# Kernel tuning notes

Hardware: AMD Instinct MI355X
Metric: run time of the kernel (lower is better)

## Reference

```python
import jax, jax.numpy as jnp
import numpy as np

N_NODES = 100000
N_EDGES = 1600000
NFEAT, NHID, NCLASS = 256, 256, 64
NLAYERS = 4


def _gcn_norm(edge_index, n_nodes):
    # PyG GCNConv default: add self-loops, symmetric normalization
    src, dst = edge_index[0], edge_index[1]
    loop = jnp.arange(n_nodes, dtype=edge_index.dtype)
    src = jnp.concatenate([src, loop])
    dst = jnp.concatenate([dst, loop])
    deg = jax.ops.segment_sum(jnp.ones_like(dst, dtype=jnp.float32), dst,
                              num_segments=n_nodes)
    dinv = jnp.where(deg > 0, jax.lax.rsqrt(deg), 0.0)
    norm = dinv[src] * dinv[dst]  # [E+N]
    return src, dst, norm


def _gcn_layer(X, W, b, src, dst, norm, n_nodes):
    H = X @ W                      # [N, out]
    msg = H[src] * norm[:, None]   # [E+N, out] gather + scale
    out = jax.ops.segment_sum(msg, dst, num_segments=n_nodes)
    return out + b


def setup_inputs() -> dict:
    key = jax.random.key(0)
    ks = jax.random.split(key, 8)
    x = jax.random.normal(ks[0], (N_NODES, NFEAT), dtype=jnp.float32)
    edge_index = jax.random.randint(ks[1], (2, N_EDGES), 0, N_NODES, dtype=jnp.int32)
    def glorot(k, fan_in, fan_out):
        s = jnp.sqrt(6.0 / (fan_in + fan_out))
        return jax.random.uniform(k, (fan_in, fan_out), jnp.float32, -s, s)
    return {
        "x": x,
        "W_enc": glorot(ks[2], NFEAT, NHID),
        "b_enc": jnp.zeros((NHID,), jnp.float32),
        "W_conv": glorot(ks[3], NHID, NHID),
        "b_conv": jnp.zeros((NHID,), jnp.float32),
        "W_dec": glorot(ks[4], NHID, NCLASS),
        "b_dec": jnp.zeros((NCLASS,), jnp.float32),
        "edge_index": edge_index,
    }


def reference(x, W_enc, b_enc, W_conv, b_conv, W_dec, b_dec, edge_index):
    n_nodes = x.shape[0]
    src, dst, norm = _gcn_norm(edge_index, n_nodes)
    # dropout probs are 0 (drop_in=drop=0) -> identity
    X = jax.nn.relu(_gcn_layer(x, W_enc, b_enc, src, dst, norm, n_nodes))
    for _ in range(NLAYERS):
        X = jax.nn.relu(_gcn_layer(X, W_conv, b_conv, src, dst, norm, n_nodes))
    X = jax.nn.relu(_gcn_layer(X, W_dec, b_dec, src, dst, norm, n_nodes))
    return X
```

## Files before the change

### kernel.cpp

```cpp
#include <hip/hip_runtime.h>

#define N_NODES 100000
#define N_EDGES 1600000
#define MPAD    100096
#define NB_SCAN ((N_NODES + 255) / 256)

using short8  = __attribute__((ext_vector_type(8))) short;
using ushort8 = __attribute__((ext_vector_type(8))) unsigned short;
using f32x4   = __attribute__((ext_vector_type(4))) float;

__device__ inline unsigned short f2bf(float f) {
    unsigned u = __float_as_uint(f);
    unsigned r = (u + 0x7fffu + ((u >> 16) & 1u)) >> 16;
    return (unsigned short)r;
}
__device__ inline float bf2f(unsigned short h) {
    return __uint_as_float(((unsigned)h) << 16);
}


__global__ __launch_bounds__(256) void k_init(int* __restrict__ indeg,
                                              int* __restrict__ cursor, int n) {
    int i = blockIdx.x * blockDim.x + threadIdx.x;
    if (i < n) { indeg[i] = 0; cursor[i] = 0; }
}

__global__ __launch_bounds__(256) void k_indeg(const int* __restrict__ dst,
                                               int* __restrict__ indeg, int e) {
    int i = blockIdx.x * blockDim.x + threadIdx.x;
    if (i < e) atomicAdd(&indeg[dst[i]], 1);
}

__global__ __launch_bounds__(256) void k_scan_blocks(const int* __restrict__ indeg,
                                                     int* __restrict__ blksum, int n) {
    int i = blockIdx.x * 256 + threadIdx.x;
    int v = (i < n) ? indeg[i] : 0;
#pragma unroll
    for (int o = 32; o > 0; o >>= 1) v += __shfl_down(v, o, 64);
    __shared__ int ws[4];
    if ((threadIdx.x & 63) == 0) ws[threadIdx.x >> 6] = v;
    __syncthreads();
    if (threadIdx.x == 0) blksum[blockIdx.x] = ws[0] + ws[1] + ws[2] + ws[3];
}

__global__ __launch_bounds__(512) void k_scan_top(const int* __restrict__ blksum,
                                                  int* __restrict__ blkpref,
                                                  int* __restrict__ offsets, int nb, int n) {
    __shared__ int s[512];
    int t = threadIdx.x;
    int v = (t < nb) ? blksum[t] : 0;
    s[t] = v;
    __syncthreads();
    for (int o = 1; o < 512; o <<= 1) {
        int u = (t >= o) ? s[t - o] : 0;
        __syncthreads();
        s[t] += u;
        __syncthreads();
    }
    if (t < nb) blkpref[t] = (t == 0) ? 0 : s[t - 1];
    if (t == nb - 1) offsets[n] = s[t];
}

__global__ __launch_bounds__(256) void k_scan_final(const int* __restrict__ indeg,
                                                    const int* __restrict__ blkpref,
                                                    int* __restrict__ offsets,
                                                    float* __restrict__ dinv, int n) {
    __shared__ int s[256];
    int t = threadIdx.x;
    int i = blockIdx.x * 256 + t;
    int v = (i < n) ? indeg[i] : 0;
    s[t] = v;
    __syncthreads();
    for (int o = 1; o < 256; o <<= 1) {
        int u = (t >= o) ? s[t - o] : 0;
        __syncthreads();
        s[t] += u;
        __syncthreads();
    }
    if (i < n) {
        offsets[i] = blkpref[blockIdx.x] + s[t] - v;
        dinv[i] = rsqrtf((float)(v + 1));
    }
}

__global__ __launch_bounds__(256) void k_scatter(const int* __restrict__ src,
                                                 const int* __restrict__ dst,
                                                 const float* __restrict__ dinv,
                                                 const int* __restrict__ offsets,
                                                 int* __restrict__ cursor,
                                                 int* __restrict__ csr_src,
                                                 float* __restrict__ csr_norm, int e) {
    int i = blockIdx.x * blockDim.x + threadIdx.x;
    if (i < e) {
        int d = dst[i], s = src[i];
        int pos = offsets[d] + atomicAdd(&cursor[d], 1);
        csr_src[pos] = s;
        csr_norm[pos] = dinv[s] * dinv[d];
    }
}


__global__ __launch_bounds__(256) void k_cvt_x(const float* __restrict__ x,
                                               unsigned short* __restrict__ xb) {
    int i = blockIdx.x * blockDim.x + threadIdx.x;
    int row = i >> 6;
    ushort4 o;
    if (row < N_NODES) {
        float4 v = *(const float4*)(x + (size_t)i * 4);
        o.x = f2bf(v.x); o.y = f2bf(v.y); o.z = f2bf(v.z); o.w = f2bf(v.w);
    } else {
        o.x = o.y = o.z = o.w = 0;
    }
    *(ushort4*)(xb + (size_t)i * 4) = o;
}

__global__ __launch_bounds__(256) void k_prep_w(const float* __restrict__ W,
                                                unsigned short* __restrict__ Wt, int N) {
    int i = blockIdx.x * blockDim.x + threadIdx.x;
    if (i < 256 * N) {
        int r = i / N, c = i - r * N;
        Wt[(size_t)c * 256 + r] = f2bf(W[i]);
    }
}


template <int BN>
__global__ __launch_bounds__(256) void k_mfma_gemm(const unsigned short* __restrict__ A,
                                                   const unsigned short* __restrict__ Bt,
                                                   unsigned short* __restrict__ C,
                                                   int Ntot) {
    constexpr int K = 256, BK = 64;
    constexpr int NFR = BN / 32;
    __shared__ char ldsA[128 * 128];
    __shared__ char ldsB[BN * 128];
    const int tid  = threadIdx.x;
    const int lane = tid & 63;
    const int wid  = tid >> 6;
    const int wr   = wid >> 1, wc = wid & 1;
    const int row0 = blockIdx.x * 128;
    const int col0 = blockIdx.y * BN;
    const int l15  = lane & 15, lhi = lane >> 4;

    f32x4 acc[4][NFR];
#pragma unroll
    for (int m = 0; m < 4; ++m)
#pragma unroll
        for (int n = 0; n < NFR; ++n) acc[m][n] = {0.f, 0.f, 0.f, 0.f};

    for (int k0 = 0; k0 < K; k0 += BK) {
#pragma unroll
        for (int j = 0; j < 4; ++j) {
            int ci = j * 256 + tid;
            int r = ci >> 3;
            int cb = (ci & 7) ^ (r & 7);
            const char* src = (const char*)(A + (size_t)(row0 + r) * K + k0) + cb * 16;
            __builtin_amdgcn_global_load_lds((const __attribute__((address_space(1))) void*)src,
                                             (__attribute__((address_space(3))) void*)(ldsA + ci * 16),
                                             16, 0, 0);
        }
#pragma unroll
        for (int j = 0; j < BN / 32; ++j) {
            int ci = j * 256 + tid;
            int r = ci >> 3;
            int cb = (ci & 7) ^ (r & 7);
            const char* src = (const char*)(Bt + (size_t)(col0 + r) * K + k0) + cb * 16;
            __builtin_amdgcn_global_load_lds((const __attribute__((address_space(1))) void*)src,
                                             (__attribute__((address_space(3))) void*)(ldsB + ci * 16),
                                             16, 0, 0);
        }
        __syncthreads();
#pragma unroll
        for (int kk = 0; kk < 2; ++kk) {
            short8 af[4], bfr[NFR];
            int cb = kk * 4 + lhi;
#pragma unroll
            for (int m = 0; m < 4; ++m) {
                int r = wr * 64 + m * 16 + l15;
                af[m] = *(const short8*)(ldsA + r * 128 + ((cb ^ (r & 7)) << 4));
            }
#pragma unroll
            for (int n = 0; n < NFR; ++n) {
                int r = wc * (NFR * 16) + n * 16 + l15;
                bfr[n] = *(const short8*)(ldsB + r * 128 + ((cb ^ (r & 7)) << 4));
            }
#pragma unroll
            for (int m = 0; m < 4; ++m)
#pragma unroll
                for (int n = 0; n < NFR; ++n)
                    acc[m][n] = __builtin_amdgcn_mfma_f32_16x16x32_bf16(af[m], bfr[n],
                                                                        acc[m][n], 0, 0, 0);
        }
        __syncthreads();
    }
#pragma unroll
    for (int m = 0; m < 4; ++m)
#pragma unroll
        for (int n = 0; n < NFR; ++n) {
            int col = col0 + wc * (NFR * 16) + n * 16 + l15;
            int rbase = row0 + wr * 64 + m * 16 + lhi * 4;
#pragma unroll
            for (int q = 0; q < 4; ++q)
                C[(size_t)(rbase + q) * Ntot + col] = f2bf(acc[m][n][q]);
        }
}


__global__ __launch_bounds__(256) void k_agg256(const unsigned short* __restrict__ H,
                                                const int* __restrict__ offsets,
                                                const int* __restrict__ csr_src,
                                                const float* __restrict__ csr_norm,
                                                const float* __restrict__ dinv,
                                                const float* __restrict__ bias,
                                                unsigned short* __restrict__ out, int n) {
    const int wid = __builtin_amdgcn_readfirstlane((blockIdx.x * blockDim.x + threadIdx.x) >> 6);
    if (wid >= n) return;
    const int lane = threadIdx.x & 63;
    const int half = lane >> 5;
    const unsigned coff = (unsigned)(lane & 31) * 16u;

    float acc[8] = {};
    const int beg = offsets[wid], end = offsets[wid + 1];
    int e = beg;

    auto do_pair = [&](int ea) {
        int s0 = csr_src[ea], s1 = csr_src[ea + 1];
        float n0 = csr_norm[ea], n1 = csr_norm[ea + 1];
        unsigned off = (unsigned)(half ? s1 : s0) * 512u + coff;
        float nrm = half ? n1 : n0;
        ushort8 v = *(const ushort8*)((const char*)H + off);
#pragma unroll
        for (int j = 0; j < 8; ++j) acc[j] = fmaf(bf2f(v[j]), nrm, acc[j]);
    };

    for (; e + 3 < end; e += 4) { do_pair(e); do_pair(e + 2); }
    for (; e + 1 < end; e += 2) { do_pair(e); }

    {
        float dv = dinv[wid];
        float sw = dv * dv;
        int  has_tail = (e < end);
        int   sA = has_tail ? csr_src[e]  : wid;
        float nA = has_tail ? csr_norm[e] : sw;
        float nB = has_tail ? sw : 0.f;
        unsigned off = (unsigned)(half ? wid : sA) * 512u + coff;
        float nrm = half ? nB : nA;
        ushort8 v = *(const ushort8*)((const char*)H + off);
#pragma unroll
        for (int j = 0; j < 8; ++j) acc[j] = fmaf(bf2f(v[j]), nrm, acc[j]);
    }

#pragma unroll
    for (int j = 0; j < 8; ++j) acc[j] += __shfl_xor(acc[j], 32);

    if (half == 0) {
        const float* bp = bias + (lane & 31) * 8;
        float4 b0 = *(const float4*)bp;
        float4 b1 = *(const float4*)(bp + 4);
        ushort8 o;
        o[0] = f2bf(fmaxf(acc[0] + b0.x, 0.f));
        o[1] = f2bf(fmaxf(acc[1] + b0.y, 0.f));
        o[2] = f2bf(fmaxf(acc[2] + b0.z, 0.f));
        o[3] = f2bf(fmaxf(acc[3] + b0.w, 0.f));
        o[4] = f2bf(fmaxf(acc[4] + b1.x, 0.f));
        o[5] = f2bf(fmaxf(acc[5] + b1.y, 0.f));
        o[6] = f2bf(fmaxf(acc[6] + b1.z, 0.f));
        o[7] = f2bf(fmaxf(acc[7] + b1.w, 0.f));
        *(ushort8*)((char*)out + (unsigned)wid * 512u + coff) = o;
    }
}


__global__ __launch_bounds__(256) void k_agg64(const unsigned short* __restrict__ H,
                                               const int* __restrict__ offsets,
                                               const int* __restrict__ csr_src,
                                               const float* __restrict__ csr_norm,
                                               const float* __restrict__ dinv,
                                               const float* __restrict__ bias,
                                               float* __restrict__ out, int n) {
    const int wid = __builtin_amdgcn_readfirstlane((blockIdx.x * blockDim.x + threadIdx.x) >> 6);
    if (wid >= n) return;
    const int lane = threadIdx.x & 63;
    const int q = lane >> 4;
    const unsigned coff = (unsigned)(lane & 15) * 8u;

    float acc[4] = {};
    const int beg = offsets[wid], end = offsets[wid + 1];
    int e = beg;

    for (; e + 3 < end; e += 4) {
        int s0 = csr_src[e], s1 = csr_src[e + 1], s2 = csr_src[e + 2], s3 = csr_src[e + 3];
        float n0 = csr_norm[e], n1 = csr_norm[e + 1], n2 = csr_norm[e + 2], n3 = csr_norm[e + 3];
        int srow = s0; float nrm = n0;
        if (q == 1) { srow = s1; nrm = n1; }
        else if (q == 2) { srow = s2; nrm = n2; }
        else if (q == 3) { srow = s3; nrm = n3; }
        ushort4 v = *(const ushort4*)((const char*)H + (unsigned)srow * 128u + coff);
        acc[0] = fmaf(bf2f(v.x), nrm, acc[0]);
        acc[1] = fmaf(bf2f(v.y), nrm, acc[1]);
        acc[2] = fmaf(bf2f(v.z), nrm, acc[2]);
        acc[3] = fmaf(bf2f(v.w), nrm, acc[3]);
    }
    {
        float dv = dinv[wid];
        float sw = dv * dv;
        int r = end - e;
        int srow = wid; float nrm = 0.f;
        if (q < r) { srow = csr_src[e + q]; nrm = csr_norm[e + q]; }
        else if (q == r) { srow = wid; nrm = sw; }
        ushort4 v = *(const ushort4*)((const char*)H + (unsigned)srow * 128u + coff);
        acc[0] = fmaf(bf2f(v.x), nrm, acc[0]);
        acc[1] = fmaf(bf2f(v.y), nrm, acc[1]);
        acc[2] = fmaf(bf2f(v.z), nrm, acc[2]);
        acc[3] = fmaf(bf2f(v.w), nrm, acc[3]);
    }
#pragma unroll
    for (int j = 0; j < 4; ++j) {
        acc[j] += __shfl_xor(acc[j], 16);
        acc[j] += __shfl_xor(acc[j], 32);
    }
    if (q == 0) {
        float4 b = *(const float4*)(bias + (lane & 15) * 4);
        float4 o = make_float4(fmaxf(acc[0] + b.x, 0.f), fmaxf(acc[1] + b.y, 0.f),
                               fmaxf(acc[2] + b.z, 0.f), fmaxf(acc[3] + b.w, 0.f));
        *(float4*)((char*)out + (size_t)wid * 256u + coff * 2u) = o;
    }
}


extern "C" void kernel_launch(void* const* d_in, const int* in_sizes, int n_in,
                              void* d_out, int out_size, void* d_ws, size_t ws_size,
                              hipStream_t stream) {
    const float* x      = (const float*)d_in[0];
    const float* W_enc  = (const float*)d_in[1];
    const float* b_enc  = (const float*)d_in[2];
    const float* W_conv = (const float*)d_in[3];
    const float* b_conv = (const float*)d_in[4];
    const float* W_dec  = (const float*)d_in[5];
    const float* b_dec  = (const float*)d_in[6];
    const int*   ei     = (const int*)d_in[7];

    const int N = N_NODES;
    const int E = N_EDGES;
    const int* src = ei;
    const int* dst = ei + E;

    size_t off = 0;
    auto carve = [&](size_t bytes) -> void* {
        void* p = (char*)d_ws + off;
        off = (off + bytes + 255) & ~(size_t)255;
        return p;
    };
    unsigned short* Xb      = (unsigned short*)carve((size_t)MPAD * 256 * 2);
    unsigned short* Hb      = (unsigned short*)carve((size_t)MPAD * 256 * 2);
    unsigned short* Wt_enc  = (unsigned short*)carve((size_t)256 * 256 * 2);
    unsigned short* Wt_conv = (unsigned short*)carve((size_t)256 * 256 * 2);
    unsigned short* Wt_dec  = (unsigned short*)carve((size_t)64 * 256 * 2);
    int*            indeg   = (int*)carve((size_t)N * sizeof(int));
    int*            cursor  = (int*)carve((size_t)N * sizeof(int));
    float*          dinv    = (float*)carve((size_t)N * sizeof(float));
    int*            offsets = (int*)carve((size_t)(N + 1) * sizeof(int));
    int*            csr_src = (int*)carve((size_t)E * sizeof(int));
    float*          csr_nrm = (float*)carve((size_t)E * sizeof(float));
    int*            blksum  = (int*)carve((size_t)NB_SCAN * sizeof(int));
    int*            blkpref = (int*)carve((size_t)NB_SCAN * sizeof(int));
    (void)ws_size;

    k_cvt_x<<<MPAD / 4, 256, 0, stream>>>(x, Xb);
    k_prep_w<<<(256 * 256 + 255) / 256, 256, 0, stream>>>(W_enc, Wt_enc, 256);
    k_prep_w<<<(256 * 256 + 255) / 256, 256, 0, stream>>>(W_conv, Wt_conv, 256);
    k_prep_w<<<(256 * 64 + 255) / 256, 256, 0, stream>>>(W_dec, Wt_dec, 64);
    k_init<<<(N + 255) / 256, 256, 0, stream>>>(indeg, cursor, N);
    k_indeg<<<(E + 255) / 256, 256, 0, stream>>>(dst, indeg, E);
    k_scan_blocks<<<NB_SCAN, 256, 0, stream>>>(indeg, blksum, N);
    k_scan_top<<<1, 512, 0, stream>>>(blksum, blkpref, offsets, NB_SCAN, N);
    k_scan_final<<<NB_SCAN, 256, 0, stream>>>(indeg, blkpref, offsets, dinv, N);
    k_scatter<<<(E + 255) / 256, 256, 0, stream>>>(src, dst, dinv, offsets, cursor,
                                                   csr_src, csr_nrm, E);

    dim3 gconv(MPAD / 128, 2);
    dim3 gdec(MPAD / 128, 1);
    const int agg_blocks = (N + 3) / 4;

    k_mfma_gemm<128><<<gconv, 256, 0, stream>>>(Xb, Wt_enc, Hb, 256);
    k_agg256<<<agg_blocks, 256, 0, stream>>>(Hb, offsets, csr_src, csr_nrm, dinv, b_enc, Xb, N);
    for (int l = 0; l < 4; ++l) {
        k_mfma_gemm<128><<<gconv, 256, 0, stream>>>(Xb, Wt_conv, Hb, 256);
        k_agg256<<<agg_blocks, 256, 0, stream>>>(Hb, offsets, csr_src, csr_nrm, dinv, b_conv, Xb, N);
    }
    k_mfma_gemm<64><<<gdec, 256, 0, stream>>>(Xb, Wt_dec, Hb, 64);
    k_agg64<<<agg_blocks, 256, 0, stream>>>(Hb, offsets, csr_src, csr_nrm, dinv, b_dec,
                                            (float*)d_out, N);
}
```

Measured before the change: 1.033 ms.

## Factor symmetric GCN norm into GEMM epilogue and aggregation, drop per-edge norm array

Splits the per-edge weight dinv[s]*dinv[d] into a row scale by dinv in the GEMM epilogue and a final scale by dinv[dst] in the aggregation. The aggregation then does plain bf16 sums and no longer reads the csr_norm array, which cuts per-edge memory traffic in every layer. The CSR scatter now decrements indeg in place instead of using a separate cursor array. The agg256 edge loop is also unrolled to issue four row gathers at once. Scaling by dinv before the bf16 rounding slightly changes numerics.

```diff
diff --git a/kernel.cpp b/kernel.cpp
--- a/kernel.cpp
+++ b/kernel.cpp
@@ -19,10 +19,9 @@
 }
 
 
-__global__ __launch_bounds__(256) void k_init(int* __restrict__ indeg,
-                                              int* __restrict__ cursor, int n) {
+__global__ __launch_bounds__(256) void k_init(int* __restrict__ indeg, int n) {
     int i = blockIdx.x * blockDim.x + threadIdx.x;
-    if (i < n) { indeg[i] = 0; cursor[i] = 0; }
+    if (i < n) indeg[i] = 0;
 }
 
 __global__ __launch_bounds__(256) void k_indeg(const int* __restrict__ dst,
@@ -85,17 +84,14 @@
 
 __global__ __launch_bounds__(256) void k_scatter(const int* __restrict__ src,
                                                  const int* __restrict__ dst,
-                                                 const float* __restrict__ dinv,
                                                  const int* __restrict__ offsets,
-                                                 int* __restrict__ cursor,
-                                                 int* __restrict__ csr_src,
-                                                 float* __restrict__ csr_norm, int e) {
+                                                 int* __restrict__ indeg,
+                                                 int* __restrict__ csr_src, int e) {
     int i = blockIdx.x * blockDim.x + threadIdx.x;
     if (i < e) {
-        int d = dst[i], s = src[i];
-        int pos = offsets[d] + atomicAdd(&cursor[d], 1);
-        csr_src[pos] = s;
-        csr_norm[pos] = dinv[s] * dinv[d];
+        int d = dst[i];
+        int pos = offsets[d] + atomicSub(&indeg[d], 1) - 1;
+        csr_src[pos] = src[i];
     }
 }
 
@@ -127,6 +123,7 @@
 template <int BN>
 __global__ __launch_bounds__(256) void k_mfma_gemm(const unsigned short* __restrict__ A,
                                                    const unsigned short* __restrict__ Bt,
+                                                   const float* __restrict__ dinv,
                                                    unsigned short* __restrict__ C,
                                                    int Ntot) {
     constexpr int K = 256, BK = 64;
@@ -193,22 +190,28 @@
         __syncthreads();
     }
 #pragma unroll
-    for (int m = 0; m < 4; ++m)
+    for (int m = 0; m < 4; ++m) {
+        int rbase = row0 + wr * 64 + m * 16 + lhi * 4;
+        float sc[4];
+#pragma unroll
+        for (int q = 0; q < 4; ++q) {
+            int grow = rbase + q;
+            sc[q] = (grow < N_NODES) ? dinv[grow] : 0.f;
+        }
 #pragma unroll
         for (int n = 0; n < NFR; ++n) {
             int col = col0 + wc * (NFR * 16) + n * 16 + l15;
-            int rbase = row0 + wr * 64 + m * 16 + lhi * 4;
 #pragma unroll
             for (int q = 0; q < 4; ++q)
-                C[(size_t)(rbase + q) * Ntot + col] = f2bf(acc[m][n][q]);
+                C[(size_t)(rbase + q) * Ntot + col] = f2bf(acc[m][n][q] * sc[q]);
         }
+    }
 }
 
 
 __global__ __launch_bounds__(256) void k_agg256(const unsigned short* __restrict__ H,
                                                 const int* __restrict__ offsets,
                                                 const int* __restrict__ csr_src,
-                                                const float* __restrict__ csr_norm,
                                                 const float* __restrict__ dinv,
                                                 const float* __restrict__ bias,
                                                 unsigned short* __restrict__ out, int n) {
@@ -222,49 +225,62 @@
     const int beg = offsets[wid], end = offsets[wid + 1];
     int e = beg;
 
-    auto do_pair = [&](int ea) {
-        int s0 = csr_src[ea], s1 = csr_src[ea + 1];
-        float n0 = csr_norm[ea], n1 = csr_norm[ea + 1];
+    for (; e + 7 < end; e += 8) {
+        int sj[8];
+#pragma unroll
+        for (int j = 0; j < 8; ++j) sj[j] = csr_src[e + j];
+        unsigned o0 = (unsigned)(half ? sj[1] : sj[0]) * 512u + coff;
+        unsigned o1 = (unsigned)(half ? sj[3] : sj[2]) * 512u + coff;
+        unsigned o2 = (unsigned)(half ? sj[5] : sj[4]) * 512u + coff;
+        unsigned o3 = (unsigned)(half ? sj[7] : sj[6]) * 512u + coff;
+        ushort8 v0 = *(const ushort8*)((const char*)H + o0);
+        ushort8 v1 = *(const ushort8*)((const char*)H + o1);
+        ushort8 v2 = *(const ushort8*)((const char*)H + o2);
+        ushort8 v3 = *(const ushort8*)((const char*)H + o3);
+#pragma unroll
+        for (int j = 0; j < 8; ++j) acc[j] += bf2f(v0[j]);
+#pragma unroll
+        for (int j = 0; j < 8; ++j) acc[j] += bf2f(v1[j]);
+#pragma unroll
+        for (int j = 0; j < 8; ++j) acc[j] += bf2f(v2[j]);
+#pragma unroll
+        for (int j = 0; j < 8; ++j) acc[j] += bf2f(v3[j]);
+    }
+    for (; e + 1 < end; e += 2) {
+        int s0 = csr_src[e], s1 = csr_src[e + 1];
         unsigned off = (unsigned)(half ? s1 : s0) * 512u + coff;
-        float nrm = half ? n1 : n0;
         ushort8 v = *(const ushort8*)((const char*)H + off);
 #pragma unroll
-        for (int j = 0; j < 8; ++j) acc[j] = fmaf(bf2f(v[j]), nrm, acc[j]);
-    };
-
-    for (; e + 3 < end; e += 4) { do_pair(e); do_pair(e + 2); }
-    for (; e + 1 < end; e += 2) { do_pair(e); }
-
+        for (int j = 0; j < 8; ++j) acc[j] += bf2f(v[j]);
+    }
     {
+        int has_tail = (e < end);
+        int sA = has_tail ? csr_src[e] : wid;
+        float wB = has_tail ? 1.f : 0.f;
+        unsigned off = (unsigned)(half ? wid : sA) * 512u + coff;
+        float w = half ? wB : 1.f;
+        ushort8 v = *(const ushort8*)((const char*)H + off);
+#pragma unroll
+        for (int j = 0; j < 8; ++j) acc[j] = fmaf(bf2f(v[j]), w, acc[j]);
+    }
+
+#pragma unroll
+    for (int j = 0; j < 8; ++j) acc[j] += __shfl_xor(acc[j], 32);
+
+    if (half == 0) {
         float dv = dinv[wid];
-        float sw = dv * dv;
-        int  has_tail = (e < end);
-        int   sA = has_tail ? csr_src[e]  : wid;
-        float nA = has_tail ? csr_norm[e] : sw;
-        float nB = has_tail ? sw : 0.f;
-        unsigned off = (unsigned)(half ? wid : sA) * 512u + coff;
-        float nrm = half ? nB : nA;
-        ushort8 v = *(const ushort8*)((const char*)H + off);
-#pragma unroll
-        for (int j = 0; j < 8; ++j) acc[j] = fmaf(bf2f(v[j]), nrm, acc[j]);
-    }
-
-#pragma unroll
-    for (int j = 0; j < 8; ++j) acc[j] += __shfl_xor(acc[j], 32);
-
-    if (half == 0) {
         const float* bp = bias + (lane & 31) * 8;
         float4 b0 = *(const float4*)bp;
         float4 b1 = *(const float4*)(bp + 4);
         ushort8 o;
-        o[0] = f2bf(fmaxf(acc[0] + b0.x, 0.f));
-        o[1] = f2bf(fmaxf(acc[1] + b0.y, 0.f));
-        o[2] = f2bf(fmaxf(acc[2] + b0.z, 0.f));
-        o[3] = f2bf(fmaxf(acc[3] + b0.w, 0.f));
-        o[4] = f2bf(fmaxf(acc[4] + b1.x, 0.f));
-        o[5] = f2bf(fmaxf(acc[5] + b1.y, 0.f));
-        o[6] = f2bf(fmaxf(acc[6] + b1.z, 0.f));
-        o[7] = f2bf(fmaxf(acc[7] + b1.w, 0.f));
+        o[0] = f2bf(fmaxf(fmaf(acc[0], dv, b0.x), 0.f));
+        o[1] = f2bf(fmaxf(fmaf(acc[1], dv, b0.y), 0.f));
+        o[2] = f2bf(fmaxf(fmaf(acc[2], dv, b0.z), 0.f));
+        o[3] = f2bf(fmaxf(fmaf(acc[3], dv, b0.w), 0.f));
+        o[4] = f2bf(fmaxf(fmaf(acc[4], dv, b1.x), 0.f));
+        o[5] = f2bf(fmaxf(fmaf(acc[5], dv, b1.y), 0.f));
+        o[6] = f2bf(fmaxf(fmaf(acc[6], dv, b1.z), 0.f));
+        o[7] = f2bf(fmaxf(fmaf(acc[7], dv, b1.w), 0.f));
         *(ushort8*)((char*)out + (unsigned)wid * 512u + coff) = o;
     }
 }
@@ -273,7 +289,6 @@
 __global__ __launch_bounds__(256) void k_agg64(const unsigned short* __restrict__ H,
                                                const int* __restrict__ offsets,
                                                const int* __restrict__ csr_src,
-                                               const float* __restrict__ csr_norm,
                                                const float* __restrict__ dinv,
                                                const float* __restrict__ bias,
                                                float* __restrict__ out, int n) {
@@ -289,29 +304,24 @@
 
     for (; e + 3 < end; e += 4) {
         int s0 = csr_src[e], s1 = csr_src[e + 1], s2 = csr_src[e + 2], s3 = csr_src[e + 3];
-        float n0 = csr_norm[e], n1 = csr_norm[e + 1], n2 = csr_norm[e + 2], n3 = csr_norm[e + 3];
-        int srow = s0; float nrm = n0;
-        if (q == 1) { srow = s1; nrm = n1; }
-        else if (q == 2) { srow = s2; nrm = n2; }
-        else if (q == 3) { srow = s3; nrm = n3; }
+        int srow = s0;
+        if (q == 1) srow = s1;
+        else if (q == 2) srow = s2;
+        else if (q == 3) srow = s3;
         ushort4 v = *(const ushort4*)((const char*)H + (unsigned)srow * 128u + coff);
-        acc[0] = fmaf(bf2f(v.x), nrm, acc[0]);
-        acc[1] = fmaf(bf2f(v.y), nrm, acc[1]);
-        acc[2] = fmaf(bf2f(v.z), nrm, acc[2]);
-        acc[3] = fmaf(bf2f(v.w), nrm, acc[3]);
+        acc[0] += bf2f(v.x); acc[1] += bf2f(v.y);
+        acc[2] += bf2f(v.z); acc[3] += bf2f(v.w);
     }
     {
-        float dv = dinv[wid];
-        float sw = dv * dv;
         int r = end - e;
-        int srow = wid; float nrm = 0.f;
-        if (q < r) { srow = csr_src[e + q]; nrm = csr_norm[e + q]; }
-        else if (q == r) { srow = wid; nrm = sw; }
+        int srow = wid; float w = 0.f;
+        if (q < r) { srow = csr_src[e + q]; w = 1.f; }
+        else if (q == r) { srow = wid; w = 1.f; }
         ushort4 v = *(const ushort4*)((const char*)H + (unsigned)srow * 128u + coff);
-        acc[0] = fmaf(bf2f(v.x), nrm, acc[0]);
-        acc[1] = fmaf(bf2f(v.y), nrm, acc[1]);
-        acc[2] = fmaf(bf2f(v.z), nrm, acc[2]);
-        acc[3] = fmaf(bf2f(v.w), nrm, acc[3]);
+        acc[0] = fmaf(bf2f(v.x), w, acc[0]);
+        acc[1] = fmaf(bf2f(v.y), w, acc[1]);
+        acc[2] = fmaf(bf2f(v.z), w, acc[2]);
+        acc[3] = fmaf(bf2f(v.w), w, acc[3]);
     }
 #pragma unroll
     for (int j = 0; j < 4; ++j) {
@@ -319,9 +329,12 @@
         acc[j] += __shfl_xor(acc[j], 32);
     }
     if (q == 0) {
+        float dv = dinv[wid];
         float4 b = *(const float4*)(bias + (lane & 15) * 4);
-        float4 o = make_float4(fmaxf(acc[0] + b.x, 0.f), fmaxf(acc[1] + b.y, 0.f),
-                               fmaxf(acc[2] + b.z, 0.f), fmaxf(acc[3] + b.w, 0.f));
+        float4 o = make_float4(fmaxf(fmaf(acc[0], dv, b.x), 0.f),
+                               fmaxf(fmaf(acc[1], dv, b.y), 0.f),
+                               fmaxf(fmaf(acc[2], dv, b.z), 0.f),
+                               fmaxf(fmaf(acc[3], dv, b.w), 0.f));
         *(float4*)((char*)out + (size_t)wid * 256u + coff * 2u) = o;
     }
 }
@@ -356,11 +369,9 @@
     unsigned short* Wt_conv = (unsigned short*)carve((size_t)256 * 256 * 2);
     unsigned short* Wt_dec  = (unsigned short*)carve((size_t)64 * 256 * 2);
     int*            indeg   = (int*)carve((size_t)N * sizeof(int));
-    int*            cursor  = (int*)carve((size_t)N * sizeof(int));
     float*          dinv    = (float*)carve((size_t)N * sizeof(float));
     int*            offsets = (int*)carve((size_t)(N + 1) * sizeof(int));
     int*            csr_src = (int*)carve((size_t)E * sizeof(int));
-    float*          csr_nrm = (float*)carve((size_t)E * sizeof(float));
     int*            blksum  = (int*)carve((size_t)NB_SCAN * sizeof(int));
     int*            blkpref = (int*)carve((size_t)NB_SCAN * sizeof(int));
     (void)ws_size;
@@ -369,25 +380,24 @@
     k_prep_w<<<(256 * 256 + 255) / 256, 256, 0, stream>>>(W_enc, Wt_enc, 256);
     k_prep_w<<<(256 * 256 + 255) / 256, 256, 0, stream>>>(W_conv, Wt_conv, 256);
     k_prep_w<<<(256 * 64 + 255) / 256, 256, 0, stream>>>(W_dec, Wt_dec, 64);
-    k_init<<<(N + 255) / 256, 256, 0, stream>>>(indeg, cursor, N);
+    k_init<<<(N + 255) / 256, 256, 0, stream>>>(indeg, N);
     k_indeg<<<(E + 255) / 256, 256, 0, stream>>>(dst, indeg, E);
     k_scan_blocks<<<NB_SCAN, 256, 0, stream>>>(indeg, blksum, N);
     k_scan_top<<<1, 512, 0, stream>>>(blksum, blkpref, offsets, NB_SCAN, N);
     k_scan_final<<<NB_SCAN, 256, 0, stream>>>(indeg, blkpref, offsets, dinv, N);
-    k_scatter<<<(E + 255) / 256, 256, 0, stream>>>(src, dst, dinv, offsets, cursor,
-                                                   csr_src, csr_nrm, E);
+    k_scatter<<<(E + 255) / 256, 256, 0, stream>>>(src, dst, offsets, indeg, csr_src, E);
 
     dim3 gconv(MPAD / 128, 2);
     dim3 gdec(MPAD / 128, 1);
     const int agg_blocks = (N + 3) / 4;
 
-    k_mfma_gemm<128><<<gconv, 256, 0, stream>>>(Xb, Wt_enc, Hb, 256);
-    k_agg256<<<agg_blocks, 256, 0, stream>>>(Hb, offsets, csr_src, csr_nrm, dinv, b_enc, Xb, N);
+    k_mfma_gemm<128><<<gconv, 256, 0, stream>>>(Xb, Wt_enc, dinv, Hb, 256);
+    k_agg256<<<agg_blocks, 256, 0, stream>>>(Hb, offsets, csr_src, dinv, b_enc, Xb, N);
     for (int l = 0; l < 4; ++l) {
-        k_mfma_gemm<128><<<gconv, 256, 0, stream>>>(Xb, Wt_conv, Hb, 256);
-        k_agg256<<<agg_blocks, 256, 0, stream>>>(Hb, offsets, csr_src, csr_nrm, dinv, b_conv, Xb, N);
-    }
-    k_mfma_gemm<64><<<gdec, 256, 0, stream>>>(Xb, Wt_dec, Hb, 64);
-    k_agg64<<<agg_blocks, 256, 0, stream>>>(Hb, offsets, csr_src, csr_nrm, dinv, b_dec,
+        k_mfma_gemm<128><<<gconv, 256, 0, stream>>>(Xb, Wt_conv, dinv, Hb, 256);
+        k_agg256<<<agg_blocks, 256, 0, stream>>>(Hb, offsets, csr_src, dinv, b_conv, Xb, N);
+    }
+    k_mfma_gemm<64><<<gdec, 256, 0, stream>>>(Xb, Wt_dec, dinv, Hb, 64);
+    k_agg64<<<agg_blocks, 256, 0, stream>>>(Hb, offsets, csr_src, dinv, b_dec,
                                             (float*)d_out, N);
 }
```

Measured after the change: 1.027 ms. Within noise of the previous version (-0.6%).
